# Kernel optimization log

Measured on AMD Instinct MI355X. Metric: run time of the kernel, lower is better.

The kernel has to match this reference:

```python
import jax, jax.numpy as jnp
import numpy as np

IN_C, HID, N_NODES, WINDOW = 8, 64, 20000, 8
N_BIG = N_NODES * WINDOW          # 160000 supernodes (window-stacked graph)
E, E_DEC = 1_600_000, 500_000
EPS = 1e-5
DH = 2 * HID + IN_C + WINDOW - 1  # 143, decoder hidden size


def _gcn(x, row, col, ew, W, b, n):
    # GCNConv with self-loops + symmetric normalization (PyG semantics)
    loop = jnp.arange(n)
    r = jnp.concatenate([row, loop])
    c = jnp.concatenate([col, loop])
    w = jnp.concatenate([ew, jnp.ones((n,), ew.dtype)])
    deg = jax.ops.segment_sum(w, c, num_segments=n)
    dis = jnp.where(deg > 0, jax.lax.rsqrt(jnp.maximum(deg, EPS)), 0.0)
    norm = dis[r] * w * dis[c]
    h = x @ W                                  # [n, HID]
    agg = jax.ops.segment_sum(norm[:, None] * h[r], c, num_segments=n)
    return agg + b


def _bn(x, g, be):
    # BatchNorm1d, training-mode batch statistics (biased var)
    m = x.mean(0)
    v = x.var(0)
    return (x - m) * jax.lax.rsqrt(v + EPS) * g + be


def _lstm(X, Wih, Whh, bih, bhh):
    # X: [T, B, F]; PyTorch gate order i,f,g,o
    Hd = Whh.shape[1]
    B = X.shape[1]

    def step(carry, xt):
        h, c = carry
        gates = xt @ Wih.T + h @ Whh.T + bih + bhh
        i, f, g, o = jnp.split(gates, 4, axis=-1)
        c = jax.nn.sigmoid(f) * c + jax.nn.sigmoid(i) * jnp.tanh(g)
        h = jax.nn.sigmoid(o) * jnp.tanh(c)
        return (h, c), h

    init = (jnp.zeros((B, Hd), X.dtype), jnp.zeros((B, Hd), X.dtype))
    (h, _), ys = jax.lax.scan(step, init, X)
    return ys, h


def setup_inputs() -> dict:
    key = jax.random.key(0)
    ks = jax.random.split(key, 20)
    f32 = jnp.float32
    sc = lambda k, shape, fan: (jax.random.normal(k, shape, f32) / np.sqrt(fan)).astype(f32)
    d = {}
    d["x"] = jax.random.normal(ks[0], (N_BIG, IN_C), f32)
    d["edge_attr"] = jax.random.uniform(ks[1], (E,), f32)
    d["edge_index"] = jax.random.randint(ks[2], (2, E), 0, N_BIG)
    d["edge_weights_index"] = jax.random.randint(ks[3], (2, E_DEC), 0, N_NODES)
    # GCN layer 1 and 2
    d["W1"] = sc(ks[4], (IN_C, HID), IN_C); d["b1"] = jnp.zeros((HID,), f32)
    d["g1"] = jnp.ones((HID,), f32); d["be1"] = jnp.zeros((HID,), f32)
    d["W2"] = sc(ks[5], (HID, HID), HID); d["b2"] = jnp.zeros((HID,), f32)
    d["g2"] = jnp.ones((HID,), f32); d["be2"] = jnp.zeros((HID,), f32)
    # LSTM 1 (input 2*HID) and LSTM 2 (input HID)
    d["Wih1"] = sc(ks[6], (4 * HID, 2 * HID), 2 * HID)
    d["Whh1"] = sc(ks[7], (4 * HID, HID), HID)
    d["bih1"] = jnp.zeros((4 * HID,), f32); d["bhh1"] = jnp.zeros((4 * HID,), f32)
    d["Wih2"] = sc(ks[8], (4 * HID, HID), HID)
    d["Whh2"] = sc(ks[9], (4 * HID, HID), HID)
    d["bih2"] = jnp.zeros((4 * HID,), f32); d["bhh2"] = jnp.zeros((4 * HID,), f32)
    # Edge decoder MLP
    d["dWa"] = sc(ks[10], (2 * DH, DH), 2 * DH); d["dba"] = jnp.zeros((DH,), f32)
    d["dWb"] = sc(ks[11], (DH, 1), DH); d["dbb"] = jnp.zeros((1,), f32)
    return d


def reference(x, edge_attr, W1, b1, g1, be1, W2, b2, g2, be2,
              Wih1, Whh1, bih1, bhh1, Wih2, Whh2, bih2, bhh2,
              dWa, dba, dWb, dbb, edge_index, edge_weights_index):
    row, col = edge_index[0], edge_index[1]
    # skip features S: first timestep full features + last channel of later steps
    Sx = x.reshape(WINDOW, N_NODES, IN_C).transpose(1, 0, 2)   # [N, W, C]
    S = jnp.concatenate([Sx[:, 0, :], Sx[:, 1:, IN_C - 1]], axis=1)  # [N, C+W-1]
    # two GCN layers (relu -> batchnorm; dropout identity in eval)
    h1 = _bn(jax.nn.relu(_gcn(x, row, col, edge_attr, W1, b1, N_BIG)), g1, be1)
    h2 = _bn(jax.nn.relu(_gcn(h1, row, col, edge_attr, W2, b2, N_BIG)), g2, be2)
    Xc = jnp.concatenate([h1, h2], axis=1).reshape(WINDOW, N_NODES, 2 * HID)
    y1, H1 = _lstm(Xc, Wih1, Whh1, bih1, bhh1)
    _, H2 = _lstm(y1, Wih2, Whh2, bih2, bhh2)
    node_emb = jnp.concatenate([H1, H2, S], axis=1)  # [N_NODES, DH]
    # edge decoder: gather-concat-MLP
    src, trg = edge_weights_index[0], edge_weights_index[1]
    ee = jnp.concatenate([node_emb[src], node_emb[trg]], axis=1)  # [E_DEC, 2*DH]
    h = jax.nn.relu(ee @ dWa + dba)
    return (h @ dWb + dbb).reshape(-1)
```

## Files before the change

### kernel.cpp

```cpp
#include <hip/hip_runtime.h>
#include <hip/hip_bf16.h>

#define IN_C 8
#define HID 64
#define N_NODES 20000
#define WINDOW 8
#define N_BIG 160000
#define NE 1600000
#define E_DEC 500000
#define DHV 143
#define EPSV 1e-5f
#define CAP 32
#define OVF_CAP 4096
#define NER 168
#define QS 16384.0f
#define IQS (1.0f / 16384.0f)

typedef __hip_bfloat16 bf;
typedef __attribute__((ext_vector_type(8))) short short8;
typedef __attribute__((ext_vector_type(4))) float float4_;

__device__ __forceinline__ float b2f(bf v) { return __bfloat162float(v); }
__device__ __forceinline__ bf f2b(float v) { return __float2bfloat16(v); }
__device__ __forceinline__ float bflo(unsigned int u) { return __uint_as_float(u << 16); }
__device__ __forceinline__ float bfhi(unsigned int u) { return __uint_as_float(u & 0xffff0000u); }
__device__ __forceinline__ unsigned int packbf2(float lo, float hi) {
    unsigned int ul = __bfloat16_as_ushort(f2b(lo));
    unsigned int uh = __bfloat16_as_ushort(f2b(hi));
    return ul | (uh << 16);
}
__device__ __forceinline__ float sigf(float x) {
    return __builtin_amdgcn_rcpf(1.f + __expf(-x));
}
__device__ __forceinline__ float tanhfast(float x) {
    x = fminf(fmaxf(x, -15.f), 15.f);
    float e = __expf(2.f * x);
    return (e - 1.f) * __builtin_amdgcn_rcpf(e + 1.f);
}

__global__ void k_prep(const float* Wih2, const float* Whh2, const float* bih1, const float* bhh1,
                       const float* bih2, const float* bhh2, const float* dWa,
                       int* cnt, int* ovfn, bf* B2f, float* bc1, float* bc2, bf* Bpqf, float* stats)
{
    int i0 = blockIdx.x * blockDim.x + threadIdx.x;
    int stride = gridDim.x * blockDim.x;
    for (int i = i0; i < N_BIG; i += stride) cnt[i] = 0;
    if (i0 == 0) *ovfn = 0;
    for (int i = i0; i < 16 * 4 * 64 * 8; i += stride) {
        int j = i & 7, lane = (i >> 3) & 63, r = i >> 9;
        int c = r & 3, ct = r >> 2;
        int q = lane >> 4, l15 = lane & 15;
        int n = ct * 16 + l15, k = c * 32 + q * 8 + j;
        B2f[i] = f2b((k < 64) ? Wih2[n * 64 + k] : Whh2[n * 64 + (k - 64)]);
    }
    for (int i = i0; i < 256; i += stride) {
        bc1[i] = bih1[i] + bhh1[i];
        bc2[i] = bih2[i] + bhh2[i];
    }
    for (int i = i0; i < 18 * 5 * 64 * 8; i += stride) {
        int j = i & 7, lane = (i >> 3) & 63, r = i >> 9;
        int c = r % 5, ct = r / 5;
        int q = lane >> 4, l15 = lane & 15;
        int n = ct * 16 + l15, k = c * 32 + q * 8 + j;
        float v = 0.f;
        if (k < DHV) {
            if (n < DHV) v = dWa[k * DHV + n];
            else if (n >= 144 && n < 144 + DHV) v = dWa[(DHV + k) * DHV + (n - 144)];
        }
        Bpqf[i] = f2b(v);
    }
    for (int i = i0; i < 256; i += stride) stats[i] = 0.f;
}

__global__ __launch_bounds__(256) void k_fill(const int* ei, const float* ea,
                                              int* cnt, unsigned int* bucket,
                                              int* ovfn, float4* ovf) {
    int e = blockIdx.x * 256 + threadIdx.x;
    int r = ei[e], c = ei[NE + e];
    float a = ea[e];
    unsigned int q = (unsigned int)(a * QS + 0.5f);
    if (q > 16383u) q = 16383u;
    int p = atomicAdd(&cnt[c], 1);
    if (p < CAP) bucket[(size_t)c * CAP + p] = ((unsigned int)r << 14) | q;
    else {
        int qq = atomicAdd(ovfn, 1);
        if (qq < OVF_CAP) ovf[qq] = make_float4(__int_as_float(c), __int_as_float(r), a, 0.f);
    }
}

__global__ __launch_bounds__(256) void k_xw1(const float* x, const float* W1, bf* hbufb) {
    __shared__ float Ws[IN_C * HID];
    __shared__ float xs[4][IN_C];
    int tid = threadIdx.x;
    Ws[tid] = W1[tid];
    Ws[tid + 256] = W1[tid + 256];
    int node0 = blockIdx.x * 4;
    if (tid < 32) xs[tid >> 3][tid & 7] = x[node0 * IN_C + tid];
    __syncthreads();
    int ch = tid & 63, ns = tid >> 6;
    float acc = 0.f;
#pragma unroll
    for (int c = 0; c < IN_C; c++) acc += xs[ns][c] * Ws[c * 64 + ch];
    hbufb[(size_t)(node0 + ns) * 64 + ch] = f2b(acc);
}

__global__ __launch_bounds__(256) void k_disscale(const int* cnt, const unsigned int* bucket,
                                                  const int* ovfn, const float4* ovf,
                                                  float* dis, bf* h) {
    int wv = (blockIdx.x * blockDim.x + threadIdx.x) >> 6;
    int half = (threadIdx.x >> 5) & 1, l = threadIdx.x & 31;
    int c = wv * 2 + half;
    if (c >= N_BIG) return;
    int n = cnt[c];
    int nb = (n < CAP) ? n : CAP;
    float s = 0.f;
    for (int i = l; i < nb; i += 32) s += (float)(bucket[(size_t)c * CAP + i] & 0x3FFFu);
    s *= IQS;
    if (n > CAP) {
        int m = *ovfn; if (m > OVF_CAP) m = OVF_CAP;
        for (int i = l; i < m; i += 32) {
            float4 v = ovf[i];
            if (__float_as_int(v.x) == c) s += v.z;
        }
    }
#pragma unroll
    for (int off = 16; off > 0; off >>= 1) s += __shfl_xor(s, off);
    float deg = 1.f + s;
    float dv = rsqrtf(fmaxf(deg, EPSV));
    if (l == 0) dis[c] = dv;
    unsigned int hv = *(const unsigned int*)(h + (size_t)c * 64 + 2 * l);
    *(unsigned int*)(h + (size_t)c * 64 + 2 * l) = packbf2(dv * bflo(hv), dv * bfhi(hv));
}

__global__ __launch_bounds__(256) void k_gcn_gather(const bf* h, const float* dis, const int* cnt,
                             const unsigned int* bucket, const int* ovfn, const float4* ovf,
                             const float* bias, bf* outb, float* part) {
    __shared__ float4 red[256];
    int tid = threadIdx.x;
    int wv = (blockIdx.x * 256 + tid) >> 6;
    int half = (tid >> 5) & 1, l = tid & 31;
    int c = wv * 2 + half;
    unsigned int hv = *(const unsigned int*)(h + (size_t)c * 64 + 2 * l);
    float ax = bflo(hv), ay = bfhi(hv);
    size_t o = (size_t)c * CAP;
    int nfull = cnt[c];
    int n = (nfull < CAP) ? nfull : CAP;
    int e = 0;
    for (; e + 8 <= n; e += 8) {
        unsigned int p[8];
#pragma unroll
        for (int j = 0; j < 8; j++) p[j] = bucket[o + e + j];
        unsigned int v[8];
#pragma unroll
        for (int j = 0; j < 8; j++)
            v[j] = *(const unsigned int*)(h + (size_t)(p[j] >> 14) * 64 + 2 * l);
#pragma unroll
        for (int j = 0; j < 8; j++) {
            float a = (float)(p[j] & 0x3FFFu) * IQS;
            ax += a * bflo(v[j]); ay += a * bfhi(v[j]);
        }
    }
    for (; e + 4 <= n; e += 4) {
        unsigned int p[4];
#pragma unroll
        for (int j = 0; j < 4; j++) p[j] = bucket[o + e + j];
        unsigned int v[4];
#pragma unroll
        for (int j = 0; j < 4; j++)
            v[j] = *(const unsigned int*)(h + (size_t)(p[j] >> 14) * 64 + 2 * l);
#pragma unroll
        for (int j = 0; j < 4; j++) {
            float a = (float)(p[j] & 0x3FFFu) * IQS;
            ax += a * bflo(v[j]); ay += a * bfhi(v[j]);
        }
    }
    for (; e < n; e++) {
        unsigned int p = bucket[o + e];
        unsigned int v = *(const unsigned int*)(h + (size_t)(p >> 14) * 64 + 2 * l);
        float a = (float)(p & 0x3FFFu) * IQS;
        ax += a * bflo(v);
        ay += a * bfhi(v);
    }
    if (nfull > CAP) {
        int m = *ovfn; if (m > OVF_CAP) m = OVF_CAP;
        for (int i = 0; i < m; i++) {
            float4 v = ovf[i];
            if (__float_as_int(v.x) == c) {
                unsigned int hw = *(const unsigned int*)(h + (size_t)__float_as_int(v.y) * 64 + 2 * l);
                ax += v.z * bflo(hw);
                ay += v.z * bfhi(hw);
            }
        }
    }
    float dv = dis[c];
    float2 bv = *(const float2*)(bias + 2 * l);
    float vx = fmaxf(dv * ax + bv.x, 0.f);
    float vy = fmaxf(dv * ay + bv.y, 0.f);
    *(unsigned int*)(outb + (size_t)c * 64 + 2 * l) = packbf2(vx, vy);
    red[tid] = make_float4(vx, vy, vx * vx, vy * vy);
    __syncthreads();
    if (tid < 32) {
        float4 s = make_float4(0.f, 0.f, 0.f, 0.f);
#pragma unroll
        for (int i = 0; i < 8; i++) {
            float4 v = red[((i >> 1) << 6) + ((i & 1) << 5) + tid];
            s.x += v.x; s.y += v.y; s.z += v.z; s.w += v.w;
        }
        float* pb = part + (size_t)blockIdx.x * 128;
        pb[2 * tid] = s.x; pb[2 * tid + 1] = s.y;
        pb[64 + 2 * tid] = s.z; pb[64 + 2 * tid + 1] = s.w;
    }
}

__global__ __launch_bounds__(256) void k_bnred(const float* part, int nblk, float* stats_out) {
    __shared__ float s[256];
    float acc = 0.f;
    for (int b = threadIdx.x; b < nblk; b += 256) acc += part[(size_t)b * 128 + blockIdx.x];
    s[threadIdx.x] = acc;
    __syncthreads();
    for (int off = 128; off; off >>= 1) {
        if (threadIdx.x < off) s[threadIdx.x] += s[threadIdx.x + off];
        __syncthreads();
    }
    if (threadIdx.x == 0) stats_out[blockIdx.x] = s[0];
}

__global__ __launch_bounds__(256) void k_fold1(const float* W2, const float* g1, const float* be1,
                                               const float* stats, bf* W2t, float* w2b, float* AC) {
    __shared__ float A[64], C[64];
    int tid = threadIdx.x;
    if (tid < 64) {
        float m = stats[tid] * (1.f / (float)N_BIG);
        float var = stats[64 + tid] * (1.f / (float)N_BIG) - m * m;
        float a = g1[tid] * rsqrtf(var + EPSV);
        float c = be1[tid] - m * a;
        A[tid] = a; C[tid] = c;
        AC[tid] = a; AC[64 + tid] = c;
    }
    __syncthreads();
    for (int i = tid; i < 4096; i += 256) {
        int n = i >> 6, k = i & 63;
        W2t[i] = f2b(W2[k * 64 + n] * A[k]);
    }
    if (tid < 64) {
        float s = 0.f;
        for (int k = 0; k < 64; k++) s += C[k] * W2[k * 64 + tid];
        w2b[tid] = s;
    }
}

__global__ void k_fold2(const float* Wih1, const float* Whh1,
                        const float* g2, const float* be2, const float* stats,
                        const float* AC, const float* bc1, bf* B1f, float* bc1f) {
    int i0 = blockIdx.x * blockDim.x + threadIdx.x;
    int stride = gridDim.x * blockDim.x;
    for (int i = i0; i < 16 * 6 * 64 * 8; i += stride) {
        int j = i & 7, lane = (i >> 3) & 63, r = i >> 9;
        int c = r % 6, ct = r / 6;
        int q = lane >> 4, l15 = lane & 15;
        int n = ct * 16 + l15, k = c * 32 + q * 8 + j;
        float w = (k < 128) ? Wih1[n * 128 + k] : Whh1[n * 64 + (k - 128)];
        float scale = 1.f;
        if (k < 64) scale = AC[k];
        else if (k < 128) {
            int ch = k - 64;
            float m = stats[128 + ch] * (1.f / (float)N_BIG);
            float var = stats[192 + ch] * (1.f / (float)N_BIG) - m * m;
            scale = g2[ch] * rsqrtf(var + EPSV);
        }
        B1f[i] = f2b(w * scale);
    }
    for (int n = i0; n < 256; n += stride) {
        float s = bc1[n];
        for (int k = 0; k < 64; k++) s += AC[64 + k] * Wih1[n * 128 + k];
        for (int ch = 0; ch < 64; ch++) {
            float m = stats[128 + ch] * (1.f / (float)N_BIG);
            float var = stats[192 + ch] * (1.f / (float)N_BIG) - m * m;
            float a = g2[ch] * rsqrtf(var + EPSV);
            float c2v = be2[ch] - m * a;
            s += c2v * Wih1[n * 128 + 64 + ch];
        }
        bc1f[n] = s;
    }
}

__global__ __launch_bounds__(256) void k_h1w2(const bf* h1b, const bf* W2t, const float* w2b,
                                              const float* dis, bf* outb) {
    int tid = threadIdx.x, w = tid >> 6, lane = tid & 63;
    int q = lane >> 4, l15 = lane & 15;
    size_t r0 = (size_t)blockIdx.x * 64 + w * 16;
    float4_ acc[4];
#pragma unroll
    for (int ct = 0; ct < 4; ct++) acc[ct] = (float4_){0.f, 0.f, 0.f, 0.f};
#pragma unroll
    for (int c = 0; c < 2; c++) {
        int koff = c * 32 + q * 8;
        short8 a = *(const short8*)(h1b + (r0 + l15) * 64 + koff);
#pragma unroll
        for (int ct = 0; ct < 4; ct++) {
            short8 b = *(const short8*)(W2t + (size_t)(ct * 16 + l15) * 64 + koff);
            acc[ct] = __builtin_amdgcn_mfma_f32_16x16x32_bf16(a, b, acc[ct], 0, 0, 0);
        }
    }
    size_t node0 = r0 + q * 4;
#pragma unroll
    for (int reg = 0; reg < 4; reg++) {
        float dv = dis[node0 + reg];
#pragma unroll
        for (int ct = 0; ct < 4; ct++)
            outb[(node0 + reg) * 64 + ct * 16 + l15] = f2b(dv * (acc[ct][reg] + w2b[ct * 16 + l15]));
    }
}

__global__ __launch_bounds__(256, 1) void k_lstm_fused(
    const bf* h1b, const bf* h2b, const bf* B1f, const bf* B2f,
    const float* bc1, const float* bc2, bf* H1out, bf* H2out)
{
    __shared__ bf h1s[2][32][72];
    __shared__ bf h2s[2][32][72];
    int tid = threadIdx.x, w = tid >> 6, lane = tid & 63;
    int q = lane >> 4, l15 = lane & 15;
    int gnode0 = blockIdx.x * 32;
    short8 B1r[6][4];
    short8 B2r[4][4];
#pragma unroll
    for (int c = 0; c < 6; c++)
#pragma unroll
        for (int g = 0; g < 4; g++)
            B1r[c][g] = *(const short8*)(B1f + (size_t)(((w + 4 * g) * 6 + c) * 64 + lane) * 8);
#pragma unroll
    for (int c = 0; c < 4; c++)
#pragma unroll
        for (int g = 0; g < 4; g++)
            B2r[c][g] = *(const short8*)(B2f + (size_t)(((w + 4 * g) * 4 + c) * 64 + lane) * 8);
    float c1[2][4] = {}, c2[2][4] = {};
    float bv1[4], bv2[4];
#pragma unroll
    for (int g = 0; g < 4; g++) {
        bv1[g] = bc1[(w + 4 * g) * 16 + l15];
        bv2[g] = bc2[(w + 4 * g) * 16 + l15];
    }
    short8 Ag[4][2], An[4][2];
#pragma unroll
    for (int c = 0; c < 4; c++) {
        const bf* sp = (c < 2) ? h1b : h2b;
        int koff = (c & 1) * 32 + q * 8;
#pragma unroll
        for (int m = 0; m < 2; m++)
            Ag[c][m] = *(const short8*)(sp + (size_t)(gnode0 + m * 16 + l15) * 64 + koff);
    }
#pragma unroll
    for (int t = 0; t < WINDOW; t++) {
        int cur = t & 1, prv = cur ^ 1;
        float4_ acc[2][4];
#pragma unroll
        for (int m = 0; m < 2; m++)
#pragma unroll
            for (int g = 0; g < 4; g++) acc[m][g] = (float4_){bv1[g], bv1[g], bv1[g], bv1[g]};
#pragma unroll
        for (int c = 0; c < 4; c++)
#pragma unroll
            for (int m = 0; m < 2; m++)
#pragma unroll
                for (int g = 0; g < 4; g++)
                    acc[m][g] = __builtin_amdgcn_mfma_f32_16x16x32_bf16(Ag[c][m], B1r[c][g], acc[m][g], 0, 0, 0);
        if (t < WINDOW - 1) {
            const size_t toff2 = (size_t)(t + 1) * N_NODES * 64;
#pragma unroll
            for (int c = 0; c < 4; c++) {
                const bf* sp = (c < 2) ? h1b + toff2 : h2b + toff2;
                int koff = (c & 1) * 32 + q * 8;
#pragma unroll
                for (int m = 0; m < 2; m++)
                    An[c][m] = *(const short8*)(sp + (size_t)(gnode0 + m * 16 + l15) * 64 + koff);
            }
        }
        if (t > 0) {
#pragma unroll
            for (int c = 4; c < 6; c++) {
                int koff = (c & 1) * 32 + q * 8;
#pragma unroll
                for (int m = 0; m < 2; m++) {
                    short8 a = *(const short8*)&h1s[prv][m * 16 + l15][koff];
#pragma unroll
                    for (int g = 0; g < 4; g++)
                        acc[m][g] = __builtin_amdgcn_mfma_f32_16x16x32_bf16(a, B1r[c][g], acc[m][g], 0, 0, 0);
                }
            }
        }
#pragma unroll
        for (int m = 0; m < 2; m++)
#pragma unroll
            for (int reg = 0; reg < 4; reg++) {
                float gi = acc[m][0][reg], gf = acc[m][1][reg];
                float gg = acc[m][2][reg], go = acc[m][3][reg];
                float co = (t == 0) ? 0.f : c1[m][reg];
                float cn = sigf(gf) * co + sigf(gi) * tanhfast(gg);
                float hn = sigf(go) * tanhfast(cn);
                c1[m][reg] = cn;
                int nl = m * 16 + q * 4 + reg;
                h1s[cur][nl][w * 16 + l15] = f2b(hn);
                if (t == WINDOW - 1)
                    H1out[(size_t)(gnode0 + nl) * 64 + w * 16 + l15] = f2b(hn);
            }
        __syncthreads();
#pragma unroll
        for (int m = 0; m < 2; m++)
#pragma unroll
            for (int g = 0; g < 4; g++) acc[m][g] = (float4_){bv2[g], bv2[g], bv2[g], bv2[g]};
#pragma unroll
        for (int c = 0; c < 2; c++) {
            int koff = (c & 1) * 32 + q * 8;
#pragma unroll
            for (int m = 0; m < 2; m++) {
                short8 a = *(const short8*)&h1s[cur][m * 16 + l15][koff];
#pragma unroll
                for (int g = 0; g < 4; g++)
                    acc[m][g] = __builtin_amdgcn_mfma_f32_16x16x32_bf16(a, B2r[c][g], acc[m][g], 0, 0, 0);
            }
        }
        if (t > 0) {
#pragma unroll
            for (int c = 2; c < 4; c++) {
                int koff = (c & 1) * 32 + q * 8;
#pragma unroll
                for (int m = 0; m < 2; m++) {
                    short8 a = *(const short8*)&h2s[prv][m * 16 + l15][koff];
#pragma unroll
                    for (int g = 0; g < 4; g++)
                        acc[m][g] = __builtin_amdgcn_mfma_f32_16x16x32_bf16(a, B2r[c][g], acc[m][g], 0, 0, 0);
                }
            }
        }
#pragma unroll
        for (int m = 0; m < 2; m++)
#pragma unroll
            for (int reg = 0; reg < 4; reg++) {
                float gi = acc[m][0][reg], gf = acc[m][1][reg];
                float gg = acc[m][2][reg], go = acc[m][3][reg];
                float co = (t == 0) ? 0.f : c2[m][reg];
                float cn = sigf(gf) * co + sigf(gi) * tanhfast(gg);
                float hn = sigf(go) * tanhfast(cn);
                c2[m][reg] = cn;
                int nl = m * 16 + q * 4 + reg;
                h2s[cur][nl][w * 16 + l15] = f2b(hn);
                if (t == WINDOW - 1)
                    H2out[(size_t)(gnode0 + nl) * 64 + w * 16 + l15] = f2b(hn);
            }
        __syncthreads();
#pragma unroll
        for (int c = 0; c < 4; c++)
#pragma unroll
            for (int m = 0; m < 2; m++) Ag[c][m] = An[c][m];
    }
}

__global__ __launch_bounds__(256) void k_pq(const bf* H1, const bf* H2, const float* x,
                                            const bf* Bpqf, const float* dba, bf* PQb) {
    __shared__ bf ne[64][NER];
    int tid = threadIdx.x, w = tid >> 6, lane = tid & 63;
    int q = lane >> 4, l15 = lane & 15;
    int r0 = blockIdx.x * 64;
    for (int i = tid; i < 64 * 16; i += 256) {
        int rr = i >> 4, cc = (i & 15) * 4;
        int gr = r0 + rr;
        uint2 v1 = make_uint2(0u, 0u), v2 = make_uint2(0u, 0u);
        if (gr < N_NODES) {
            v1 = *(const uint2*)(H1 + (size_t)gr * 64 + cc);
            v2 = *(const uint2*)(H2 + (size_t)gr * 64 + cc);
        }
        *(uint2*)&ne[rr][cc] = v1;
        *(uint2*)&ne[rr][64 + cc] = v2;
    }
    for (int i = tid; i < 64 * 32; i += 256) {
        int rr = i >> 5, cc = 128 + (i & 31);
        int gr = r0 + rr;
        float v = 0.f;
        if (gr < N_NODES && cc < DHV) {
            int s = cc - 128;
            v = (s < 8) ? x[gr * IN_C + s] : x[(size_t)((s - 7) * N_NODES + gr) * IN_C + 7];
        }
        ne[rr][cc] = f2b(v);
    }
    __syncthreads();
    float4_ acc[18];
#pragma unroll
    for (int ct = 0; ct < 18; ct++) acc[ct] = (float4_){0.f, 0.f, 0.f, 0.f};
#pragma unroll
    for (int c = 0; c < 5; c++) {
        short8 a = *(const short8*)&ne[w * 16 + l15][c * 32 + q * 8];
#pragma unroll
        for (int ct = 0; ct < 18; ct++) {
            short8 b = *(const short8*)(Bpqf + (size_t)((ct * 5 + c) * 64 + lane) * 8);
            acc[ct] = __builtin_amdgcn_mfma_f32_16x16x32_bf16(a, b, acc[ct], 0, 0, 0);
        }
    }
#pragma unroll
    for (int reg = 0; reg < 4; reg++) {
        int nrow = r0 + w * 16 + q * 4 + reg;
        if (nrow < N_NODES)
#pragma unroll
            for (int ct = 0; ct < 18; ct++) {
                int col = ct * 16 + l15;
                float add = (ct < 9 && col < DHV) ? dba[col] : 0.f;
                PQb[(size_t)nrow * 288 + col] = f2b(acc[ct][reg] + add);
            }
    }
}

__global__ __launch_bounds__(256) void k_edge(const int* ewi, const bf* PQb,
                                              const float* dWb, const float* dbb, float* out) {
    int wv = (blockIdx.x * blockDim.x + threadIdx.x) >> 6;
    int half = (threadIdx.x >> 5) & 1, l = threadIdx.x & 31;
    int e = wv * 2 + half;
    if (e >= E_DEC) return;
    int src = ewi[e], trg = ewi[E_DEC + e];
    const bf* Pr = PQb + (size_t)src * 288;
    const bf* Qr = PQb + (size_t)trg * 288 + 144;
    float acc;
    {
        uint2 pv = *(const uint2*)(Pr + 4 * l);
        uint2 qv = *(const uint2*)(Qr + 4 * l);
        float4 wv4 = *(const float4*)(dWb + 4 * l);
        float s0 = fmaxf(bflo(pv.x) + bflo(qv.x), 0.f);
        float s1 = fmaxf(bfhi(pv.x) + bfhi(qv.x), 0.f);
        float s2 = fmaxf(bflo(pv.y) + bflo(qv.y), 0.f);
        float s3 = fmaxf(bfhi(pv.y) + bfhi(qv.y), 0.f);
        acc = s0 * wv4.x + s1 * wv4.y + s2 * wv4.z + s3 * wv4.w;
    }
    if (l < 4) {
        int u0 = 128 + 4 * l;
        uint2 pv = *(const uint2*)(Pr + u0);
        uint2 qv = *(const uint2*)(Qr + u0);
        float w0 = dWb[u0], w1 = dWb[u0 + 1], w2 = dWb[u0 + 2];
        float w3 = (u0 + 3 < DHV) ? dWb[u0 + 3] : 0.f;
        acc += fmaxf(bflo(pv.x) + bflo(qv.x), 0.f) * w0;
        acc += fmaxf(bfhi(pv.x) + bfhi(qv.x), 0.f) * w1;
        acc += fmaxf(bflo(pv.y) + bflo(qv.y), 0.f) * w2;
        acc += fmaxf(bfhi(pv.y) + bfhi(qv.y), 0.f) * w3;
    }
#pragma unroll
    for (int off = 16; off > 0; off >>= 1) acc += __shfl_xor(acc, off);
    if (l == 0) out[e] = acc + dbb[0];
}

extern "C" void kernel_launch(void* const* d_in, const int* in_sizes, int n_in,
                              void* d_out, int out_size, void* d_ws, size_t ws_size,
                              hipStream_t stream) {
    (void)in_sizes; (void)n_in; (void)out_size; (void)ws_size;
    const float* x    = (const float*)d_in[0];
    const float* ea   = (const float*)d_in[1];
    const int*   ei   = (const int*)d_in[2];
    const int*   ewi  = (const int*)d_in[3];
    const float* W1   = (const float*)d_in[4];
    const float* b1   = (const float*)d_in[5];
    const float* g1   = (const float*)d_in[6];
    const float* be1  = (const float*)d_in[7];
    const float* W2   = (const float*)d_in[8];
    const float* b2   = (const float*)d_in[9];
    const float* g2   = (const float*)d_in[10];
    const float* be2  = (const float*)d_in[11];
    const float* Wih1 = (const float*)d_in[12];
    const float* Whh1 = (const float*)d_in[13];
    const float* bih1 = (const float*)d_in[14];
    const float* bhh1 = (const float*)d_in[15];
    const float* Wih2 = (const float*)d_in[16];
    const float* Whh2 = (const float*)d_in[17];
    const float* bih2 = (const float*)d_in[18];
    const float* bhh2 = (const float*)d_in[19];
    const float* dWa  = (const float*)d_in[20];
    const float* dba  = (const float*)d_in[21];
    const float* dWb  = (const float*)d_in[22];
    const float* dbb  = (const float*)d_in[23];
    float* out = (float*)d_out;

    const size_t NSB = (size_t)N_BIG * 64;
    const size_t NS  = (size_t)N_NODES * 64;
    char* base = (char*)d_ws;
    size_t o = 0;
    float* dis  = (float*)(base + o); o += (size_t)N_BIG * 4;
    bf* PQb     = (bf*)(base + o);    o += NSB * 2;
    bf* hbufb   = (bf*)(base + o);    o += NSB * 2;
    bf* h1b     = (bf*)(base + o);    o += NSB * 2;
    bf* h2b     = (bf*)(base + o);    o += NSB * 2;
    bf* hs1     = (bf*)(base + o);    o += NS * 2;
    bf* hs2     = (bf*)(base + o);    o += NS * 2;
    bf* B1f     = (bf*)(base + o);    o += (size_t)16 * 6 * 64 * 8 * 2;
    bf* B2f     = (bf*)(base + o);    o += (size_t)16 * 4 * 64 * 8 * 2;
    bf* W2t     = (bf*)(base + o);    o += 64 * 64 * 2;
    float* bc1  = (float*)(base + o); o += 256 * 4;
    float* bc2  = (float*)(base + o); o += 256 * 4;
    bf* Bpqf    = (bf*)(base + o);    o += (size_t)18 * 5 * 64 * 8 * 2;
    float* stats= (float*)(base + o); o += 256 * 4;
    float* w2b  = (float*)(base + o); o += 64 * 4;
    float* AC   = (float*)(base + o); o += 128 * 4;
    float* bc1f = (float*)(base + o); o += 256 * 4;
    int* cnt    = (int*)(base + o);   o += (size_t)N_BIG * 4;
    int* ovfn   = (int*)(base + o);   o += 256;
    float4* ovf = (float4*)(base + o); o += (size_t)OVF_CAP * 16;
    unsigned int* bucket = (unsigned int*)(base + o); o += (size_t)N_BIG * CAP * 4;
    float* part = (float*)(base + o); o += (size_t)20000 * 128 * 4;

    k_prep<<<512, 256, 0, stream>>>(Wih2, Whh2, bih1, bhh1, bih2, bhh2, dWa,
                                    cnt, ovfn, B2f, bc1, bc2, Bpqf, stats);
    k_fill<<<6250, 256, 0, stream>>>(ei, ea, cnt, bucket, ovfn, ovf);
    k_xw1<<<N_BIG / 4, 256, 0, stream>>>(x, W1, hbufb);
    k_disscale<<<N_BIG / 8, 256, 0, stream>>>(cnt, bucket, ovfn, ovf, dis, hbufb);

    k_gcn_gather<<<N_BIG / 8, 256, 0, stream>>>(hbufb, dis, cnt, bucket, ovfn, ovf, b1, h1b, part);
    k_bnred<<<128, 256, 0, stream>>>(part, 20000, stats);
    k_fold1<<<1, 256, 0, stream>>>(W2, g1, be1, stats, W2t, w2b, AC);

    k_h1w2<<<2500, 256, 0, stream>>>(h1b, W2t, w2b, dis, hbufb);
    k_gcn_gather<<<N_BIG / 8, 256, 0, stream>>>(hbufb, dis, cnt, bucket, ovfn, ovf, b2, h2b, part);
    k_bnred<<<128, 256, 0, stream>>>(part, 20000, stats + 128);
    k_fold2<<<64, 256, 0, stream>>>(Wih1, Whh1, g2, be2, stats, AC, bc1, B1f, bc1f);

    k_lstm_fused<<<625, 256, 0, stream>>>(h1b, h2b, B1f, B2f, bc1f, bc2, hs1, hs2);

    k_pq<<<313, 256, 0, stream>>>(hs1, hs2, x, Bpqf, dba, PQb);
    k_edge<<<E_DEC / 8, 256, 0, stream>>>(ewi, PQb, dWb, dbb, out);
}
```

Before: 619.9 us.

## Fuse prep with edge fill and xW1 with degree scaling, memset counters

The weight-prep kernel and the edge-bucket fill kernel become one launch, with blocks split by blockIdx. The x@W1 projection is computed inside the degree/dis kernel, so the unscaled hbuf is never written and read back. Counter zeroing moves to a hipMemsetAsync, and fold2 now sums the biases itself because bc1 may not be ready. This removes two launches and one global round trip of the 160000x64 bf16 buffer. Stats zeroing is dropped, which seems safe only if bnred overwrites stats rather than accumulating into them.

```diff
diff --git a/kernel.cpp b/kernel.cpp
--- a/kernel.cpp
+++ b/kernel.cpp
@@ -38,14 +38,29 @@
     return (e - 1.f) * __builtin_amdgcn_rcpf(e + 1.f);
 }
 
-__global__ void k_prep(const float* Wih2, const float* Whh2, const float* bih1, const float* bhh1,
-                       const float* bih2, const float* bhh2, const float* dWa,
-                       int* cnt, int* ovfn, bf* B2f, float* bc1, float* bc2, bf* Bpqf, float* stats)
+__global__ __launch_bounds__(256) void k_prepfill(
+    const int* ei, const float* ea, int* cnt, unsigned int* bucket, int* ovfn, float4* ovf,
+    const float* Wih2, const float* Whh2, const float* bih1, const float* bhh1,
+    const float* bih2, const float* bhh2, const float* dWa,
+    bf* B2f, float* bc1, float* bc2, bf* Bpqf)
 {
-    int i0 = blockIdx.x * blockDim.x + threadIdx.x;
-    int stride = gridDim.x * blockDim.x;
-    for (int i = i0; i < N_BIG; i += stride) cnt[i] = 0;
-    if (i0 == 0) *ovfn = 0;
+    int tid = threadIdx.x;
+    if (blockIdx.x < 6250) {
+        int e = blockIdx.x * 256 + tid;
+        int r = ei[e], c = ei[NE + e];
+        float a = ea[e];
+        unsigned int q = (unsigned int)(a * QS + 0.5f);
+        if (q > 16383u) q = 16383u;
+        int p = atomicAdd(&cnt[c], 1);
+        if (p < CAP) bucket[(size_t)c * CAP + p] = ((unsigned int)r << 14) | q;
+        else {
+            int qq = atomicAdd(ovfn, 1);
+            if (qq < OVF_CAP) ovf[qq] = make_float4(__int_as_float(c), __int_as_float(r), a, 0.f);
+        }
+        return;
+    }
+    int i0 = (blockIdx.x - 6250) * 256 + tid;
+    int stride = 512 * 256;
     for (int i = i0; i < 16 * 4 * 64 * 8; i += stride) {
         int j = i & 7, lane = (i >> 3) & 63, r = i >> 9;
         int c = r & 3, ct = r >> 2;
@@ -69,52 +84,26 @@
         }
         Bpqf[i] = f2b(v);
     }
-    for (int i = i0; i < 256; i += stride) stats[i] = 0.f;
-}
-
-__global__ __launch_bounds__(256) void k_fill(const int* ei, const float* ea,
-                                              int* cnt, unsigned int* bucket,
-                                              int* ovfn, float4* ovf) {
-    int e = blockIdx.x * 256 + threadIdx.x;
-    int r = ei[e], c = ei[NE + e];
-    float a = ea[e];
-    unsigned int q = (unsigned int)(a * QS + 0.5f);
-    if (q > 16383u) q = 16383u;
-    int p = atomicAdd(&cnt[c], 1);
-    if (p < CAP) bucket[(size_t)c * CAP + p] = ((unsigned int)r << 14) | q;
-    else {
-        int qq = atomicAdd(ovfn, 1);
-        if (qq < OVF_CAP) ovf[qq] = make_float4(__int_as_float(c), __int_as_float(r), a, 0.f);
-    }
-}
-
-__global__ __launch_bounds__(256) void k_xw1(const float* x, const float* W1, bf* hbufb) {
-    __shared__ float Ws[IN_C * HID];
-    __shared__ float xs[4][IN_C];
+}
+
+__global__ __launch_bounds__(256) void k_xw1dis(const float* x, const float* W1,
+        const int* cnt, const unsigned int* bucket, const int* ovfn, const float4* ovf,
+        float* dis, bf* hbufb) {
+    __shared__ float Ws[8][64];
+    __shared__ float xs[8][8];
     int tid = threadIdx.x;
-    Ws[tid] = W1[tid];
-    Ws[tid + 256] = W1[tid + 256];
-    int node0 = blockIdx.x * 4;
-    if (tid < 32) xs[tid >> 3][tid & 7] = x[node0 * IN_C + tid];
+    Ws[tid >> 6][tid & 63] = W1[tid];
+    Ws[4 + (tid >> 6)][tid & 63] = W1[256 + tid];
+    int nb0 = blockIdx.x * 8;
+    if (tid < 64) xs[tid >> 3][tid & 7] = x[nb0 * IN_C + tid];
     __syncthreads();
-    int ch = tid & 63, ns = tid >> 6;
-    float acc = 0.f;
-#pragma unroll
-    for (int c = 0; c < IN_C; c++) acc += xs[ns][c] * Ws[c * 64 + ch];
-    hbufb[(size_t)(node0 + ns) * 64 + ch] = f2b(acc);
-}
-
-__global__ __launch_bounds__(256) void k_disscale(const int* cnt, const unsigned int* bucket,
-                                                  const int* ovfn, const float4* ovf,
-                                                  float* dis, bf* h) {
-    int wv = (blockIdx.x * blockDim.x + threadIdx.x) >> 6;
-    int half = (threadIdx.x >> 5) & 1, l = threadIdx.x & 31;
-    int c = wv * 2 + half;
-    if (c >= N_BIG) return;
+    int wv = tid >> 6, half = (tid >> 5) & 1, l = tid & 31;
+    int nl = wv * 2 + half;
+    int c = nb0 + nl;
     int n = cnt[c];
-    int nb = (n < CAP) ? n : CAP;
+    int nbk = (n < CAP) ? n : CAP;
     float s = 0.f;
-    for (int i = l; i < nb; i += 32) s += (float)(bucket[(size_t)c * CAP + i] & 0x3FFFu);
+    for (int i = l; i < nbk; i += 32) s += (float)(bucket[(size_t)c * CAP + i] & 0x3FFFu);
     s *= IQS;
     if (n > CAP) {
         int m = *ovfn; if (m > OVF_CAP) m = OVF_CAP;
@@ -125,11 +114,16 @@
     }
 #pragma unroll
     for (int off = 16; off > 0; off >>= 1) s += __shfl_xor(s, off);
-    float deg = 1.f + s;
-    float dv = rsqrtf(fmaxf(deg, EPSV));
+    float dv = rsqrtf(fmaxf(1.f + s, EPSV));
     if (l == 0) dis[c] = dv;
-    unsigned int hv = *(const unsigned int*)(h + (size_t)c * 64 + 2 * l);
-    *(unsigned int*)(h + (size_t)c * 64 + 2 * l) = packbf2(dv * bflo(hv), dv * bfhi(hv));
+    float a0 = 0.f, a1 = 0.f;
+#pragma unroll
+    for (int k = 0; k < IN_C; k++) {
+        float xv = xs[nl][k];
+        a0 += xv * Ws[k][2 * l];
+        a1 += xv * Ws[k][2 * l + 1];
+    }
+    *(unsigned int*)(hbufb + (size_t)c * 64 + 2 * l) = packbf2(dv * a0, dv * a1);
 }
 
 __global__ __launch_bounds__(256) void k_gcn_gather(const bf* h, const float* dis, const int* cnt,
@@ -251,7 +245,8 @@
 
 __global__ void k_fold2(const float* Wih1, const float* Whh1,
                         const float* g2, const float* be2, const float* stats,
-                        const float* AC, const float* bc1, bf* B1f, float* bc1f) {
+                        const float* AC, const float* bih1, const float* bhh1,
+                        bf* B1f, float* bc1f) {
     int i0 = blockIdx.x * blockDim.x + threadIdx.x;
     int stride = gridDim.x * blockDim.x;
     for (int i = i0; i < 16 * 6 * 64 * 8; i += stride) {
@@ -271,7 +266,7 @@
         B1f[i] = f2b(w * scale);
     }
     for (int n = i0; n < 256; n += stride) {
-        float s = bc1[n];
+        float s = bih1[n] + bhh1[n];
         for (int k = 0; k < 64; k++) s += AC[64 + k] * Wih1[n * 128 + k];
         for (int ch = 0; ch < 64; ch++) {
             float m = stats[128 + ch] * (1.f / (float)N_BIG);
@@ -588,24 +583,24 @@
     bf* B1f     = (bf*)(base + o);    o += (size_t)16 * 6 * 64 * 8 * 2;
     bf* B2f     = (bf*)(base + o);    o += (size_t)16 * 4 * 64 * 8 * 2;
     bf* W2t     = (bf*)(base + o);    o += 64 * 64 * 2;
+    bf* Bpqf    = (bf*)(base + o);    o += (size_t)18 * 5 * 64 * 8 * 2;
     float* bc1  = (float*)(base + o); o += 256 * 4;
     float* bc2  = (float*)(base + o); o += 256 * 4;
-    bf* Bpqf    = (bf*)(base + o);    o += (size_t)18 * 5 * 64 * 8 * 2;
     float* stats= (float*)(base + o); o += 256 * 4;
     float* w2b  = (float*)(base + o); o += 64 * 4;
     float* AC   = (float*)(base + o); o += 128 * 4;
     float* bc1f = (float*)(base + o); o += 256 * 4;
     int* cnt    = (int*)(base + o);   o += (size_t)N_BIG * 4;
-    int* ovfn   = (int*)(base + o);   o += 256;
+    int* ovfn   = (int*)(base + o);   o += 256 * 4;
     float4* ovf = (float4*)(base + o); o += (size_t)OVF_CAP * 16;
     unsigned int* bucket = (unsigned int*)(base + o); o += (size_t)N_BIG * CAP * 4;
     float* part = (float*)(base + o); o += (size_t)20000 * 128 * 4;
 
-    k_prep<<<512, 256, 0, stream>>>(Wih2, Whh2, bih1, bhh1, bih2, bhh2, dWa,
-                                    cnt, ovfn, B2f, bc1, bc2, Bpqf, stats);
-    k_fill<<<6250, 256, 0, stream>>>(ei, ea, cnt, bucket, ovfn, ovf);
-    k_xw1<<<N_BIG / 4, 256, 0, stream>>>(x, W1, hbufb);
-    k_disscale<<<N_BIG / 8, 256, 0, stream>>>(cnt, bucket, ovfn, ovf, dis, hbufb);
+    hipMemsetAsync(cnt, 0, ((size_t)N_BIG + 256) * 4, stream);
+    k_prepfill<<<6250 + 512, 256, 0, stream>>>(ei, ea, cnt, bucket, ovfn, ovf,
+                                               Wih2, Whh2, bih1, bhh1, bih2, bhh2, dWa,
+                                               B2f, bc1, bc2, Bpqf);
+    k_xw1dis<<<N_BIG / 8, 256, 0, stream>>>(x, W1, cnt, bucket, ovfn, ovf, dis, hbufb);
 
     k_gcn_gather<<<N_BIG / 8, 256, 0, stream>>>(hbufb, dis, cnt, bucket, ovfn, ovf, b1, h1b, part);
     k_bnred<<<128, 256, 0, stream>>>(part, 20000, stats);
@@ -614,7 +609,7 @@
     k_h1w2<<<2500, 256, 0, stream>>>(h1b, W2t, w2b, dis, hbufb);
     k_gcn_gather<<<N_BIG / 8, 256, 0, stream>>>(hbufb, dis, cnt, bucket, ovfn, ovf, b2, h2b, part);
     k_bnred<<<128, 256, 0, stream>>>(part, 20000, stats + 128);
-    k_fold2<<<64, 256, 0, stream>>>(Wih1, Whh1, g2, be2, stats, AC, bc1, B1f, bc1f);
+    k_fold2<<<64, 256, 0, stream>>>(Wih1, Whh1, g2, be2, stats, AC, bih1, bhh1, B1f, bc1f);
 
     k_lstm_fused<<<625, 256, 0, stream>>>(h1b, h2b, B1f, B2f, bc1f, bc2, hs1, hs2);
 
```

After: 613.7 us. No clear change (-1.0%).
